# Performance work log

Hardware: AMD Instinct MI355X
Metric: run time of the kernel (lower is better)

## Reference

```python
import jax, jax.numpy as jnp
import numpy as np
import string

N_QUBITS = 16
N_LAYERS = 2
BATCH = 32
DIM = 2 ** N_QUBITS


def _apply_1q(psi, U, q):
    # psi: (B,) + (2,)*n complex; U: (2,2) complex acting on qubit q
    n = psi.ndim - 1
    ax = string.ascii_lowercase[:n]
    out = list(ax)
    out[q] = 'A'
    return jnp.einsum('A' + ax[q] + ',z' + ax + '->z' + ''.join(out), U, psi)


def _apply_2q(psi, G, c, t):
    # G: (2,2,2,2) = (out_c, out_t, in_c, in_t)
    n = psi.ndim - 1
    ax = string.ascii_lowercase[:n]
    out = list(ax)
    out[c] = 'A'
    out[t] = 'B'
    return jnp.einsum('AB' + ax[c] + ax[t] + ',z' + ax + '->z' + ''.join(out), G, psi)


def _rx(th):
    c = jnp.cos(th * 0.5).astype(jnp.complex64)
    s = jnp.sin(th * 0.5).astype(jnp.complex64)
    return jnp.array([[c, -1j * s], [-1j * s, c]])


def _ry(th):
    c = jnp.cos(th * 0.5).astype(jnp.complex64)
    s = jnp.sin(th * 0.5).astype(jnp.complex64)
    return jnp.array([[c, -s], [s, c]])


def _rz(th):
    th_c = th.astype(jnp.complex64)
    z = jnp.zeros((), jnp.complex64)
    return jnp.array([[jnp.exp(-0.5j * th_c), z], [z, jnp.exp(0.5j * th_c)]])


_CNOT = jnp.array([[1, 0, 0, 0],
                   [0, 1, 0, 0],
                   [0, 0, 0, 1],
                   [0, 0, 1, 0]], dtype=jnp.complex64).reshape(2, 2, 2, 2)


def setup_inputs() -> dict:
    key = jax.random.key(0)
    k1, k2, k3 = jax.random.split(key, 3)
    thetas = jax.random.normal(k1, (N_LAYERS, 3, N_QUBITS), dtype=jnp.float32)
    re = jax.random.normal(k2, (BATCH, DIM), dtype=jnp.float32)
    im = jax.random.normal(k3, (BATCH, DIM), dtype=jnp.float32)
    norm = jnp.sqrt(jnp.sum(re * re + im * im, axis=-1, keepdims=True))
    return {"thetas": thetas, "state_re": re / norm, "state_im": im / norm}


def reference(thetas, state_re, state_im):
    B = state_re.shape[0]
    psi = (state_re.astype(jnp.complex64) + 1j * state_im.astype(jnp.complex64))
    psi = psi.reshape((B,) + (2,) * N_QUBITS)
    for l in range(N_LAYERS):
        for q in range(N_QUBITS):
            psi = _apply_1q(psi, _rx(thetas[l, 0, q]), q)
            psi = _apply_1q(psi, _ry(thetas[l, 1, q]), q)
            psi = _apply_1q(psi, _rz(thetas[l, 2, q]), q)
        for q in range(N_QUBITS):
            psi = _apply_2q(psi, _CNOT, q, (q + 1) % N_QUBITS)
    probs = (psi.real ** 2 + psi.imag ** 2).reshape(B, -1)
    return probs
```

## Files before the change

### kernel.cpp

```cpp
#include <hip/hip_runtime.h>


#define NT 256

__device__ __forceinline__ int fperm(int x) {
  int y = x ^ (x >> 1);
  y ^= (x & 1) ? 0xC000 : 0;
  return y & 0xFFFF;
}

__device__ __forceinline__ int finv16(int x) {
  int s = x;
  s ^= s >> 1; s ^= s >> 2; s ^= s >> 4; s ^= s >> 8;
  int b15 = ((s ^ (s >> 15)) & 1) << 15;
  return (s & 0x7FFF) | b15;
}

__device__ __forceinline__ int swz(int l) { return l ^ ((l >> 4) & 15); }

__device__ __forceinline__ void compute_gates(const float* __restrict__ th, float* gsh) {
  int tid = threadIdx.x;
  if (tid < 32) {
    int l = tid >> 4, q = tid & 15;
    float tx = th[l * 48 + q], ty = th[l * 48 + 16 + q], tz = th[l * 48 + 32 + q];
    float cx, sx, cy, sy, cz, sz;
    sincosf(0.5f * tx, &sx, &cx);
    sincosf(0.5f * ty, &sy, &cy);
    sincosf(0.5f * tz, &sz, &cz);
    float m00r = cy * cx, m00i =  sy * sx;
    float m01r = -sy * cx, m01i = -cy * sx;
    float m10r =  sy * cx, m10i = -cy * sx;
    float m11r =  cy * cx, m11i = -sy * sx;
    float* G = gsh + tid * 8;
    G[0] = cz * m00r + sz * m00i;  G[1] = cz * m00i - sz * m00r;
    G[2] = cz * m01r + sz * m01i;  G[3] = cz * m01i - sz * m01r;
    G[4] = cz * m10r - sz * m10i;  G[5] = cz * m10i + sz * m10r;
    G[6] = cz * m11r - sz * m11i;  G[7] = cz * m11i + sz * m11r;
  }
}

template <int MK, int SK, int N>
__device__ __forceinline__ void greg(float2 (&a)[N], const float* G, int c) {
  const float4* G4 = (const float4*)G;
  float4 r0 = G4[0], r1 = G4[1];
  bool sw = (c != 0);
  float h00r = sw ? r1.z : r0.x, h00i = sw ? r1.w : r0.y;
  float h01r = sw ? r1.x : r0.z, h01i = sw ? r1.y : r0.w;
  float h10r = sw ? r0.z : r1.x, h10i = sw ? r0.w : r1.y;
  float h11r = sw ? r0.x : r1.z, h11i = sw ? r0.y : r1.w;
  constexpr int PV = MK & (-MK);
#pragma unroll
  for (int k = 0; k < N; k++) {
    if (k & PV) continue;
    const int k2 = k ^ MK;
    const int p0 = __builtin_popcount(k & SK) & 1;
    const int ka = p0 ? k2 : k;
    const int kb = p0 ? k : k2;
    float2 x = a[ka], y = a[kb];
    a[ka] = make_float2(h00r * x.x - h00i * x.y + h01r * y.x - h01i * y.y,
                        h00r * x.y + h00i * x.x + h01r * y.y + h01i * y.x);
    a[kb] = make_float2(h10r * x.x - h10i * x.y + h11r * y.x - h11i * y.y,
                        h10r * x.y + h10i * x.x + h11r * y.y + h11i * y.x);
  }
}


__device__ __forceinline__ void phaseA_body(int t, int bbase, int wb,
                                            const float* gsh, float2* samp,
                                            const float* __restrict__ xre,
                                            const float* __restrict__ xim,
                                            float2* __restrict__ ws) {
  float2 a[16];
  int base = bbase + (wb << 12);
  const float4* xr4 = (const float4*)(xre + base + (t << 4));
  const float4* xi4 = (const float4*)(xim + base + (t << 4));
#pragma unroll
  for (int q = 0; q < 4; q++) {
    float4 v = xr4[q], w = xi4[q];
    a[4*q+0] = make_float2(v.x, w.x); a[4*q+1] = make_float2(v.y, w.y);
    a[4*q+2] = make_float2(v.z, w.z); a[4*q+3] = make_float2(v.w, w.w);
  }
  __syncthreads();
  greg<1, 1>(a, gsh + 15 * 8, 0);
  greg<2, 2>(a, gsh + 14 * 8, 0);
  greg<4, 4>(a, gsh + 13 * 8, 0);
  greg<8, 8>(a, gsh + 12 * 8, 0);
#pragma unroll
  for (int k = 0; k < 16; k++) samp[swz((t << 4) | k)] = a[k];
  __syncthreads();
#pragma unroll
  for (int k = 0; k < 16; k++)
    a[k] = samp[swz((t & 15) | (k << 4) | ((t >> 4) << 8))];
  greg<1, 1>(a, gsh + 11 * 8, 0);
  greg<2, 2>(a, gsh + 10 * 8, 0);
  greg<4, 4>(a, gsh + 9 * 8, 0);
  greg<8, 8>(a, gsh + 8 * 8, 0);
#pragma unroll
  for (int k = 0; k < 16; k++)
    samp[swz((t & 15) | (k << 4) | ((t >> 4) << 8))] = a[k];
  __syncthreads();
#pragma unroll
  for (int k = 0; k < 16; k++) a[k] = samp[swz(t | (k << 8))];
  greg<1, 1>(a, gsh + 7 * 8, 0);
  greg<2, 2>(a, gsh + 6 * 8, 0);
  greg<4, 4>(a, gsh + 5 * 8, 0);
  greg<8, 8>(a, gsh + 4 * 8, 0);
#pragma unroll
  for (int k = 0; k < 16; k++)
    ws[base + t + (k << 8)] = a[k];
}

__device__ __forceinline__ void phaseB_body(int t, int bbase, int wb,
                                            const float* gsh, float2* samp,
                                            float2* __restrict__ ws) {
  float2 a[16];
#pragma unroll
  for (int k = 0; k < 16; k++)
    a[k] = ws[bbase + t + (wb << 8) + (k << 12)];
  int cA = (__popc(t) + __popc(wb)) & 1;
  greg<1, 1>(a, gsh + 3 * 8, 0);
  greg<2, 2>(a, gsh + 2 * 8, 0);
  greg<4, 4>(a, gsh + 1 * 8, 0);
  greg<8, 8>(a, gsh + 0 * 8, 0);
  greg<12, 7>(a, gsh + (16 + 0) * 8, cA);
  greg<6, 12>(a, gsh + (16 + 1) * 8, 0);
  greg<3, 14>(a, gsh + (16 + 2) * 8, 0);
  __syncthreads();
#pragma unroll
  for (int k = 0; k < 16; k++) samp[swz(t | (k << 8))] = a[k];
  __syncthreads();
#pragma unroll
  for (int k = 0; k < 16; k++)
    a[k] = samp[swz((k & 3) | (t << 2) | ((k >> 2) << 10))];
  greg<13, 15>(a, gsh + (16 + 15) * 8, cA);
  greg<3, 14>(a, gsh + (16 + 14) * 8, cA);
#pragma unroll
  for (int k = 0; k < 16; k++)
    samp[swz((k & 3) | (t << 2) | ((k >> 2) << 10))] = a[k];
  __syncthreads();
#pragma unroll
  for (int k = 0; k < 16; k++)
    a[k] = samp[swz((t & 1) | (k << 1) | ((t >> 1) << 5))];
  {
    int cC = (__popc(t >> 1) + __popc(wb)) & 1;
    greg<3, 14>(a, gsh + (16 + 13) * 8, cC);
    greg<6, 12>(a, gsh + (16 + 12) * 8, cC);
    greg<12, 8>(a, gsh + (16 + 11) * 8, cC);
  }
#pragma unroll
  for (int k = 0; k < 16; k++)
    samp[swz((t & 1) | (k << 1) | ((t >> 1) << 5))] = a[k];
  __syncthreads();
#pragma unroll
  for (int k = 0; k < 16; k++)
    a[k] = samp[swz((t & 15) | (k << 4) | ((t >> 4) << 8))];
  {
    int cD = (__popc(t >> 4) + __popc(wb)) & 1;
    greg<3, 14>(a, gsh + (16 + 10) * 8, cD);
    greg<6, 12>(a, gsh + (16 + 9) * 8, cD);
    greg<12, 8>(a, gsh + (16 + 8) * 8, cD);
  }
#pragma unroll
  for (int k = 0; k < 16; k++) {
    int full = (t & 15) | (k << 4) | (wb << 8) | ((t >> 4) << 12);
    ws[bbase + full] = a[k];
  }
}

__device__ __forceinline__ void phaseC_body(int t, int bbase, int wb,
                                            const float* gsh, float2* samp,
                                            const float2* __restrict__ ws,
                                            float* __restrict__ out) {
  int fix = ((wb & 1) << 7) | ((wb >> 1) << 13);
  int jt = (t & 127) | ((t >> 7) << 8) | fix;
  float2 a[16];
#pragma unroll
  for (int k = 0; k < 16; k++) {
    int j = jt | (k << 9);
    a[k] = ws[bbase + fperm(j)];
  }
  greg<1, 1>(a, gsh + (16 + 6) * 8, 0);
  greg<2, 2>(a, gsh + (16 + 5) * 8, 0);
  greg<4, 4>(a, gsh + (16 + 4) * 8, 0);
  greg<8, 8>(a, gsh + (16 + 3) * 8, 0);
#pragma unroll
  for (int k = 0; k < 16; k++) samp[swz(t | (k << 8))] = a[k];
  __syncthreads();
#pragma unroll
  for (int k = 0; k < 16; k++)
    a[k] = samp[swz((t & 127) | (k << 7) | ((t >> 7) << 11))];
  greg<1, 1>(a, gsh + (16 + 7) * 8, 0);
#pragma unroll
  for (int k = 0; k < 16; k++) {
    int l = (t & 127) | (k << 7) | ((t >> 7) << 11);
    int j = (l & 127) | (((l >> 7) & 1) << 8) | ((l >> 8) << 9) | fix;
    out[bbase + finv16(j)] = a[k].x * a[k].x + a[k].y * a[k].y;
  }
}


__global__ void __launch_bounds__(NT, 2) pass1_k(const float* __restrict__ th,
                                                 const float* __restrict__ xre,
                                                 const float* __restrict__ xim,
                                                 float2* __restrict__ ws) {
  __shared__ float gsh[256];
  __shared__ float2 samp[4096];
  int t = threadIdx.x, blk = blockIdx.x;
  int batch = (blk & 7) + ((blk >> 7) << 3), wb = (blk >> 3) & 15;
  compute_gates(th, gsh);
  phaseA_body(t, batch << 16, wb, gsh, samp, xre, xim, ws);
}

__global__ void __launch_bounds__(NT, 2) pass2_k(const float* __restrict__ th,
                                                 float2* __restrict__ ws) {
  __shared__ float gsh[256];
  __shared__ float2 samp[4096];
  int t = threadIdx.x, blk = blockIdx.x;
  int batch = (blk & 7) + ((blk >> 7) << 3), wb = (blk >> 3) & 15;
  compute_gates(th, gsh);
  __syncthreads();
  phaseB_body(t, batch << 16, wb, gsh, samp, ws);
}

__global__ void __launch_bounds__(NT, 2) pass3_k(const float* __restrict__ th,
                                                 const float2* __restrict__ ws,
                                                 float* __restrict__ out) {
  __shared__ float gsh[256];
  __shared__ float2 samp[4096];
  int t = threadIdx.x, blk = blockIdx.x;
  int batch = (blk & 7) + ((blk >> 7) << 3), wb = (blk >> 3) & 15;
  compute_gates(th, gsh);
  __syncthreads();
  phaseC_body(t, batch << 16, wb, gsh, samp, ws, out);
}


__device__ __forceinline__ void signal(unsigned* cnt) {
  __threadfence();
  __syncthreads();
  if (threadIdx.x == 0)
    __hip_atomic_fetch_add(cnt, 1u, __ATOMIC_RELEASE, __HIP_MEMORY_SCOPE_AGENT);
}

__device__ __forceinline__ void wait16(unsigned* cnt) {
  if (threadIdx.x == 0) {
    while (__hip_atomic_load(cnt, __ATOMIC_ACQUIRE, __HIP_MEMORY_SCOPE_AGENT) < 16u)
      __builtin_amdgcn_s_sleep(2);
  }
  __syncthreads();
  __threadfence();
}

__global__ void __launch_bounds__(NT, 2)
fused_k(const float* __restrict__ th,
        const float* __restrict__ xre, const float* __restrict__ xim,
        float2* __restrict__ ws, float* __restrict__ out,
        unsigned* __restrict__ cnt1, unsigned* __restrict__ cnt2) {
  __shared__ float gsh[256];
  __shared__ float2 samp[4096];
  int t = threadIdx.x, blk = blockIdx.x;
  int batch = (blk & 7) + ((blk >> 7) << 3), wb = (blk >> 3) & 15;
  int bbase = batch << 16;

  compute_gates(th, gsh);
  phaseA_body(t, bbase, wb, gsh, samp, xre, xim, ws);
  signal(&cnt1[batch << 5]);

  wait16(&cnt1[batch << 5]);
  phaseB_body(t, bbase, wb, gsh, samp, ws);
  signal(&cnt2[batch << 5]);

  wait16(&cnt2[batch << 5]);
  phaseC_body(t, bbase, wb, gsh, samp, ws, out);
}


extern "C" void kernel_launch(void* const* d_in, const int* in_sizes, int n_in,
                              void* d_out, int out_size, void* d_ws, size_t ws_size,
                              hipStream_t stream) {
  const float* th  = (const float*)d_in[0];
  const float* xre = (const float*)d_in[1];
  const float* xim = (const float*)d_in[2];
  float* out = (float*)d_out;

  float2* amp = (float2*)d_ws;
  unsigned* cnt1 = (unsigned*)((char*)d_ws + (16u << 20));
  unsigned* cnt2 = cnt1 + 1024;

  int maxBlk = 0;
  hipError_t qrc = hipOccupancyMaxActiveBlocksPerMultiprocessor(
      &maxBlk, (const void*)fused_k, NT, 0);
  bool try_coop = (qrc == hipSuccess && maxBlk >= 2);

  bool coop_ok = false;
  if (try_coop) {
    hipMemsetAsync((void*)cnt1, 0, 2048 * sizeof(unsigned), stream);
    void* args[] = {(void*)&th, (void*)&xre, (void*)&xim,
                    (void*)&amp, (void*)&out, (void*)&cnt1, (void*)&cnt2};
    hipError_t rc = hipLaunchCooperativeKernel((const void*)fused_k, dim3(512),
                                               dim3(NT), args, 0, stream);
    coop_ok = (rc == hipSuccess);
  }

  if (!coop_ok) {
    pass1_k<<<512, NT, 0, stream>>>(th, xre, xim, amp);
    pass2_k<<<512, NT, 0, stream>>>(th, amp);
    pass3_k<<<512, NT, 0, stream>>>(th, amp, out);
  }
}
```

Before: 106.8 us.

## Store intermediate amplitudes in fp16 and replace cooperative fused kernel with three launches

Intermediate state amplitudes between passes are stored as half2 instead of float2, halving workspace traffic. The cooperative fused kernel with atomic counters, the memset and the occupancy query is removed in favour of three plain kernel launches. Global loads are issued before gate computation to overlap latency, and output stores are made nontemporal. fp16 storage risks accuracy loss against the reference tolerance.

```diff
diff --git a/kernel.cpp b/kernel.cpp
--- a/kernel.cpp
+++ b/kernel.cpp
@@ -1,4 +1,5 @@
 #include <hip/hip_runtime.h>
+#include <hip/hip_fp16.h>
 
 
 #define NT 256
@@ -17,6 +18,13 @@
 }
 
 __device__ __forceinline__ int swz(int l) { return l ^ ((l >> 4) & 15); }
+
+__device__ __forceinline__ __half2 packa(float2 a) {
+  return __floats2half2_rn(a.x, a.y);
+}
+__device__ __forceinline__ float2 unpacka(__half2 h) {
+  return __half22float2(h);
+}
 
 __device__ __forceinline__ void compute_gates(const float* __restrict__ th, float* gsh) {
   int tid = threadIdx.x;
@@ -65,11 +73,15 @@
 }
 
 
-__device__ __forceinline__ void phaseA_body(int t, int bbase, int wb,
-                                            const float* gsh, float2* samp,
-                                            const float* __restrict__ xre,
-                                            const float* __restrict__ xim,
-                                            float2* __restrict__ ws) {
+__global__ void __launch_bounds__(NT, 2) pass1_k(const float* __restrict__ th,
+                                                 const float* __restrict__ xre,
+                                                 const float* __restrict__ xim,
+                                                 __half2* __restrict__ ws) {
+  __shared__ float gsh[256];
+  __shared__ float2 samp[4096];
+  int t = threadIdx.x, blk = blockIdx.x;
+  int batch = (blk & 7) + ((blk >> 7) << 3), wb = (blk >> 3) & 15;
+  int bbase = batch << 16;
   float2 a[16];
   int base = bbase + (wb << 12);
   const float4* xr4 = (const float4*)(xre + base + (t << 4));
@@ -80,6 +92,7 @@
     a[4*q+0] = make_float2(v.x, w.x); a[4*q+1] = make_float2(v.y, w.y);
     a[4*q+2] = make_float2(v.z, w.z); a[4*q+3] = make_float2(v.w, w.w);
   }
+  compute_gates(th, gsh);
   __syncthreads();
   greg<1, 1>(a, gsh + 15 * 8, 0);
   greg<2, 2>(a, gsh + 14 * 8, 0);
@@ -107,16 +120,23 @@
   greg<8, 8>(a, gsh + 4 * 8, 0);
 #pragma unroll
   for (int k = 0; k < 16; k++)
-    ws[base + t + (k << 8)] = a[k];
-}
-
-__device__ __forceinline__ void phaseB_body(int t, int bbase, int wb,
-                                            const float* gsh, float2* samp,
-                                            float2* __restrict__ ws) {
+    ws[base + t + (k << 8)] = packa(a[k]);
+}
+
+
+__global__ void __launch_bounds__(NT, 2) pass2_k(const float* __restrict__ th,
+                                                 __half2* __restrict__ ws) {
+  __shared__ float gsh[256];
+  __shared__ float2 samp[4096];
+  int t = threadIdx.x, blk = blockIdx.x;
+  int batch = (blk & 7) + ((blk >> 7) << 3), wb = (blk >> 3) & 15;
+  int bbase = batch << 16;
   float2 a[16];
 #pragma unroll
   for (int k = 0; k < 16; k++)
-    a[k] = ws[bbase + t + (wb << 8) + (k << 12)];
+    a[k] = unpacka(ws[bbase + t + (wb << 8) + (k << 12)]);
+  compute_gates(th, gsh);
+  __syncthreads();
   int cA = (__popc(t) + __popc(wb)) & 1;
   greg<1, 1>(a, gsh + 3 * 8, 0);
   greg<2, 2>(a, gsh + 2 * 8, 0);
@@ -125,7 +145,6 @@
   greg<12, 7>(a, gsh + (16 + 0) * 8, cA);
   greg<6, 12>(a, gsh + (16 + 1) * 8, 0);
   greg<3, 14>(a, gsh + (16 + 2) * 8, 0);
-  __syncthreads();
 #pragma unroll
   for (int k = 0; k < 16; k++) samp[swz(t | (k << 8))] = a[k];
   __syncthreads();
@@ -163,115 +182,47 @@
 #pragma unroll
   for (int k = 0; k < 16; k++) {
     int full = (t & 15) | (k << 4) | (wb << 8) | ((t >> 4) << 12);
-    ws[bbase + full] = a[k];
-  }
-}
-
-__device__ __forceinline__ void phaseC_body(int t, int bbase, int wb,
-                                            const float* gsh, float2* samp,
-                                            const float2* __restrict__ ws,
-                                            float* __restrict__ out) {
-  int fix = ((wb & 1) << 7) | ((wb >> 1) << 13);
-  int jt = (t & 127) | ((t >> 7) << 8) | fix;
-  float2 a[16];
-#pragma unroll
-  for (int k = 0; k < 16; k++) {
-    int j = jt | (k << 9);
-    a[k] = ws[bbase + fperm(j)];
-  }
-  greg<1, 1>(a, gsh + (16 + 6) * 8, 0);
-  greg<2, 2>(a, gsh + (16 + 5) * 8, 0);
-  greg<4, 4>(a, gsh + (16 + 4) * 8, 0);
-  greg<8, 8>(a, gsh + (16 + 3) * 8, 0);
-#pragma unroll
-  for (int k = 0; k < 16; k++) samp[swz(t | (k << 8))] = a[k];
-  __syncthreads();
-#pragma unroll
-  for (int k = 0; k < 16; k++)
-    a[k] = samp[swz((t & 127) | (k << 7) | ((t >> 7) << 11))];
-  greg<1, 1>(a, gsh + (16 + 7) * 8, 0);
-#pragma unroll
-  for (int k = 0; k < 16; k++) {
-    int l = (t & 127) | (k << 7) | ((t >> 7) << 11);
-    int j = (l & 127) | (((l >> 7) & 1) << 8) | ((l >> 8) << 9) | fix;
-    out[bbase + finv16(j)] = a[k].x * a[k].x + a[k].y * a[k].y;
-  }
-}
-
-
-__global__ void __launch_bounds__(NT, 2) pass1_k(const float* __restrict__ th,
-                                                 const float* __restrict__ xre,
-                                                 const float* __restrict__ xim,
-                                                 float2* __restrict__ ws) {
-  __shared__ float gsh[256];
-  __shared__ float2 samp[4096];
-  int t = threadIdx.x, blk = blockIdx.x;
-  int batch = (blk & 7) + ((blk >> 7) << 3), wb = (blk >> 3) & 15;
-  compute_gates(th, gsh);
-  phaseA_body(t, batch << 16, wb, gsh, samp, xre, xim, ws);
-}
-
-__global__ void __launch_bounds__(NT, 2) pass2_k(const float* __restrict__ th,
-                                                 float2* __restrict__ ws) {
-  __shared__ float gsh[256];
-  __shared__ float2 samp[4096];
-  int t = threadIdx.x, blk = blockIdx.x;
-  int batch = (blk & 7) + ((blk >> 7) << 3), wb = (blk >> 3) & 15;
-  compute_gates(th, gsh);
-  __syncthreads();
-  phaseB_body(t, batch << 16, wb, gsh, samp, ws);
-}
+    ws[bbase + full] = packa(a[k]);
+  }
+}
+
 
 __global__ void __launch_bounds__(NT, 2) pass3_k(const float* __restrict__ th,
-                                                 const float2* __restrict__ ws,
+                                                 const __half2* __restrict__ ws,
                                                  float* __restrict__ out) {
   __shared__ float gsh[256];
   __shared__ float2 samp[4096];
   int t = threadIdx.x, blk = blockIdx.x;
   int batch = (blk & 7) + ((blk >> 7) << 3), wb = (blk >> 3) & 15;
+  int bbase = batch << 16;
+  int fix = ((wb & 1) << 7) | ((wb >> 1) << 13);
+  int jt = (t & 127) | ((t >> 7) << 8) | fix;
+  float2 a[16];
+#pragma unroll
+  for (int k = 0; k < 16; k++) {
+    int j = jt | (k << 9);
+    a[k] = unpacka(ws[bbase + fperm(j)]);
+  }
   compute_gates(th, gsh);
   __syncthreads();
-  phaseC_body(t, batch << 16, wb, gsh, samp, ws, out);
-}
-
-
-__device__ __forceinline__ void signal(unsigned* cnt) {
-  __threadfence();
-  __syncthreads();
-  if (threadIdx.x == 0)
-    __hip_atomic_fetch_add(cnt, 1u, __ATOMIC_RELEASE, __HIP_MEMORY_SCOPE_AGENT);
-}
-
-__device__ __forceinline__ void wait16(unsigned* cnt) {
-  if (threadIdx.x == 0) {
-    while (__hip_atomic_load(cnt, __ATOMIC_ACQUIRE, __HIP_MEMORY_SCOPE_AGENT) < 16u)
-      __builtin_amdgcn_s_sleep(2);
-  }
-  __syncthreads();
-  __threadfence();
-}
-
-__global__ void __launch_bounds__(NT, 2)
-fused_k(const float* __restrict__ th,
-        const float* __restrict__ xre, const float* __restrict__ xim,
-        float2* __restrict__ ws, float* __restrict__ out,
-        unsigned* __restrict__ cnt1, unsigned* __restrict__ cnt2) {
-  __shared__ float gsh[256];
-  __shared__ float2 samp[4096];
-  int t = threadIdx.x, blk = blockIdx.x;
-  int batch = (blk & 7) + ((blk >> 7) << 3), wb = (blk >> 3) & 15;
-  int bbase = batch << 16;
-
-  compute_gates(th, gsh);
-  phaseA_body(t, bbase, wb, gsh, samp, xre, xim, ws);
-  signal(&cnt1[batch << 5]);
-
-  wait16(&cnt1[batch << 5]);
-  phaseB_body(t, bbase, wb, gsh, samp, ws);
-  signal(&cnt2[batch << 5]);
-
-  wait16(&cnt2[batch << 5]);
-  phaseC_body(t, bbase, wb, gsh, samp, ws, out);
+  greg<1, 1>(a, gsh + (16 + 6) * 8, 0);
+  greg<2, 2>(a, gsh + (16 + 5) * 8, 0);
+  greg<4, 4>(a, gsh + (16 + 4) * 8, 0);
+  greg<8, 8>(a, gsh + (16 + 3) * 8, 0);
+#pragma unroll
+  for (int k = 0; k < 16; k++) samp[swz(t | (k << 8))] = a[k];
+  __syncthreads();
+#pragma unroll
+  for (int k = 0; k < 16; k++)
+    a[k] = samp[swz((t & 127) | (k << 7) | ((t >> 7) << 11))];
+  greg<1, 1>(a, gsh + (16 + 7) * 8, 0);
+#pragma unroll
+  for (int k = 0; k < 16; k++) {
+    int l = (t & 127) | (k << 7) | ((t >> 7) << 11);
+    int j = (l & 127) | (((l >> 7) & 1) << 8) | ((l >> 8) << 9) | fix;
+    float pr = a[k].x * a[k].x + a[k].y * a[k].y;
+    __builtin_nontemporal_store(pr, &out[bbase + finv16(j)]);
+  }
 }
 
 
@@ -283,28 +234,9 @@
   const float* xim = (const float*)d_in[2];
   float* out = (float*)d_out;
 
-  float2* amp = (float2*)d_ws;
-  unsigned* cnt1 = (unsigned*)((char*)d_ws + (16u << 20));
-  unsigned* cnt2 = cnt1 + 1024;
-
-  int maxBlk = 0;
-  hipError_t qrc = hipOccupancyMaxActiveBlocksPerMultiprocessor(
-      &maxBlk, (const void*)fused_k, NT, 0);
-  bool try_coop = (qrc == hipSuccess && maxBlk >= 2);
-
-  bool coop_ok = false;
-  if (try_coop) {
-    hipMemsetAsync((void*)cnt1, 0, 2048 * sizeof(unsigned), stream);
-    void* args[] = {(void*)&th, (void*)&xre, (void*)&xim,
-                    (void*)&amp, (void*)&out, (void*)&cnt1, (void*)&cnt2};
-    hipError_t rc = hipLaunchCooperativeKernel((const void*)fused_k, dim3(512),
-                                               dim3(NT), args, 0, stream);
-    coop_ok = (rc == hipSuccess);
-  }
-
-  if (!coop_ok) {
-    pass1_k<<<512, NT, 0, stream>>>(th, xre, xim, amp);
-    pass2_k<<<512, NT, 0, stream>>>(th, amp);
-    pass3_k<<<512, NT, 0, stream>>>(th, amp, out);
-  }
-}
+  __half2* amp = (__half2*)d_ws;
+
+  pass1_k<<<512, NT, 0, stream>>>(th, xre, xim, amp);
+  pass2_k<<<512, NT, 0, stream>>>(th, amp);
+  pass3_k<<<512, NT, 0, stream>>>(th, amp, out);
+}
```

Result: faster. 104.5 us (-2.1%).
